# Kernel tuning notes

Hardware: AMD Instinct MI355X
Metric: run time of the kernel (lower is better)

The kernel has to match this reference:

```python
import jax, jax.numpy as jnp
import numpy as np

N, IN_DIM, OUT_DIM, H = 1024, 128, 128, 4
D = OUT_DIM // H  # head_dim = 32
NEG_SLOPE = 0.2
MASK_VAL = -1e9
LN_EPS = 1e-5


def setup_inputs() -> dict:
    key = jax.random.key(0)
    k = jax.random.split(key, 8)
    h = jax.random.normal(k[0], (N, IN_DIM), dtype=jnp.float32)
    adj = jax.random.randint(k[1], (N, N), 0, 2, dtype=jnp.int32)
    adj = adj.at[jnp.arange(N), jnp.arange(N)].set(1)  # self-loops
    s = 1.0 / np.sqrt(IN_DIM)
    W_l = jax.random.normal(k[2], (IN_DIM, OUT_DIM), dtype=jnp.float32) * s
    W_r = jax.random.normal(k[3], (IN_DIM, OUT_DIM), dtype=jnp.float32) * s
    W_v = jax.random.normal(k[4], (IN_DIM, OUT_DIM), dtype=jnp.float32) * s
    a = jax.random.normal(k[5], (D,), dtype=jnp.float32) * (1.0 / np.sqrt(D))
    ln_g = jnp.ones((OUT_DIM,), dtype=jnp.float32)
    ln_b = jnp.zeros((OUT_DIM,), dtype=jnp.float32)
    return {"h": h, "adj": adj, "W_l": W_l, "W_r": W_r, "W_v": W_v,
            "a": a, "ln_g": ln_g, "ln_b": ln_b}


def reference(h, adj, W_l, W_r, W_v, a, ln_g, ln_b):
    n = h.shape[0]
    Wlh = (h @ W_l).reshape(n, H, D)   # [N,H,D]
    Wrh = (h @ W_r).reshape(n, H, D)   # [N,H,D]
    # pairwise additive scores: pair[i,j,h,d] = Wlh[i] + Wrh[j]
    pair = Wlh[:, None, :, :] + Wrh[None, :, :, :]          # [N,N,H,D]
    pair = jnp.where(pair >= 0, pair, NEG_SLOPE * pair)      # leaky_relu(0.2)
    e = jnp.einsum('ijhd,d->ijh', pair, a)                   # [N,N,H]
    mask = (adj != 0)[:, :, None]                            # [N,N,1]
    e = jnp.where(mask, e, MASK_VAL)
    alpha = jax.nn.softmax(e, axis=1)                        # softmax over j
    v = (h @ W_v).reshape(n, H, D)                           # [N,H,D]
    agg = jnp.einsum('ijh,jhd->ihd', alpha, v).reshape(n, OUT_DIM)
    mu = jnp.mean(agg, axis=-1, keepdims=True)
    var = jnp.mean((agg - mu) ** 2, axis=-1, keepdims=True)
    y = (agg - mu) * jax.lax.rsqrt(var + LN_EPS) * ln_g + ln_b
    return jax.nn.relu(y)
```

## Files before the change

kernel.cpp:

```cpp
#include <hip/hip_runtime.h>

typedef _Float16 f16;
typedef _Float16 f16x2 __attribute__((ext_vector_type(2)));
typedef _Float16 f16x4 __attribute__((ext_vector_type(4)));
typedef _Float16 f16x8 __attribute__((ext_vector_type(8)));
typedef float    f32x4 __attribute__((ext_vector_type(4)));
typedef unsigned int u32;

#define LOG2E 1.44269504088896340736f

__device__ __forceinline__ f16x2 habs2(f16x2 v) {
    union { f16x2 h; u32 u; } x; x.h = v; x.u &= 0x7FFF7FFFu; return x.h;
}
#if __has_builtin(__builtin_amdgcn_fdot2)
__device__ __forceinline__ float fdot2f(f16x2 a, f16x2 b, float c) {
    return __builtin_amdgcn_fdot2(a, b, c, false);
}
#else
__device__ __forceinline__ float fdot2f(f16x2 a, f16x2 b, float c) {
    return c + (float)a.x * (float)b.x + (float)a.y * (float)b.y;
}
#endif
#if __has_builtin(__builtin_amdgcn_exp2f)
#define EXP2F __builtin_amdgcn_exp2f
#else
#define EXP2F exp2f
#endif

__global__ __launch_bounds__(384) void k1_proj(
        const float* __restrict__ h,  const float* __restrict__ Wl,
        const float* __restrict__ Wr, const float* __restrict__ Wv,
        f16* __restrict__ Wlh, f16* __restrict__ WrL, f16* __restrict__ VL) {
    __shared__ float hs[2][128];
    const int t = threadIdx.x, i0 = blockIdx.x * 2;
    if (t < 256) hs[t >> 7][t & 127] = h[(i0 + (t >> 7)) * 128 + (t & 127)];
    __syncthreads();

    const int wsel = t >> 7, col = t & 127;
    const float* W = (wsel == 0) ? Wl : ((wsel == 1) ? Wr : Wv);
    float a0 = 0.f, a1 = 0.f;
    #pragma unroll 16
    for (int k = 0; k < 128; k++) {
        float wv = W[k * 128 + col];
        a0 += hs[0][k] * wv;
        a1 += hs[1][k] * wv;
    }
    float accs[2] = {a0, a1};
    const int hh = col >> 5, dd = col & 31, c = dd >> 2, l = dd & 3;
    #pragma unroll
    for (int i = 0; i < 2; i++) {
        int j = i0 + i;
        f16 hv = (f16)accs[i];
        if (wsel == 0)      Wlh[j * 128 + col] = hv;
        else if (wsel == 1) WrL[((hh * 8 + c) * 1024 + j) * 4 + l] = hv;
        else                VL[(hh * 32 + dd) * 1024 + j] = hv;
    }
}

__global__ __launch_bounds__(256) void GATv2Layer_84447646974220_kernel(
        const f16* __restrict__ Wlh, const f16* __restrict__ WrL,
        const f16* __restrict__ VL,  const int* __restrict__ adj,
        const float* __restrict__ a_, const float* __restrict__ ln_g,
        const float* __restrict__ ln_b, float* __restrict__ out) {

    __shared__ __align__(16) f16 ep[4][2][1024];
    __shared__ float aggS[2][4][32];

    const int t    = threadIdx.x;
    const int lane = t & 63;
    const int hh   = t >> 6;
    const int i0   = blockIdx.x * 2;

    f16x2 p2[16], q2[16];
    #pragma unroll
    for (int d2 = 0; d2 < 16; d2++) {
        float a0 = a_[2 * d2], a1 = a_[2 * d2 + 1];
        f16x2 p; p.x = (f16)(0.6f * a0); p.y = (f16)(0.6f * a1);
        f16x2 q; q.x = (f16)(0.4f * a0); q.y = (f16)(0.4f * a1);
        p2[d2] = p; q2[d2] = q;
    }
    f16x2 wl2[2][16];
    #pragma unroll
    for (int ii = 0; ii < 2; ii++) {
        const f16x2* src = (const f16x2*)(Wlh + (i0 + ii) * 128 + hh * 32);
        #pragma unroll
        for (int c2 = 0; c2 < 16; c2++) wl2[ii][c2] = src[c2];
    }

    float maxE[2] = {-__builtin_inff(), -__builtin_inff()};
    f16x4 wrA[8], wrB[8];
    int   amA[2], amB[2];

    #pragma unroll
    for (int c = 0; c < 8; c++)
        wrA[c] = *(const f16x4*)(WrL + ((hh * 8 + c) * 1024 + lane) * 4);
    amA[0] = adj[(i0 + 0) * 1024 + lane];
    amA[1] = adj[(i0 + 1) * 1024 + lane];

    #pragma unroll
    for (int jb = 0; jb < 16; jb++) {
        const bool even = (jb & 1) == 0;
        f16x4* cur = even ? wrA : wrB;
        int*   amc = even ? amA : amB;
        f16x4* nxt = even ? wrB : wrA;
        int*   amn = even ? amB : amA;
        if (jb < 15) {
            int jn = (jb + 1) * 64 + lane;
            #pragma unroll
            for (int c = 0; c < 8; c++)
                nxt[c] = *(const f16x4*)(WrL + ((hh * 8 + c) * 1024 + jn) * 4);
            amn[0] = adj[(i0 + 0) * 1024 + jn];
            amn[1] = adj[(i0 + 1) * 1024 + jn];
        }
        int j = jb * 64 + lane;
        float e[2] = {0.f, 0.f};
        #pragma unroll
        for (int c = 0; c < 8; c++) {
            #pragma unroll
            for (int ii = 0; ii < 2; ii++) {
                f16x2 t0 = wl2[ii][2 * c]     + cur[c].lo;
                f16x2 t1 = wl2[ii][2 * c + 1] + cur[c].hi;
                e[ii] = fdot2f(p2[2 * c],     t0, e[ii]);
                e[ii] = fdot2f(q2[2 * c],     habs2(t0), e[ii]);
                e[ii] = fdot2f(p2[2 * c + 1], t1, e[ii]);
                e[ii] = fdot2f(q2[2 * c + 1], habs2(t1), e[ii]);
            }
        }
        #pragma unroll
        for (int ii = 0; ii < 2; ii++) {
            float v = amc[ii] ? e[ii] : -__builtin_inff();
            maxE[ii] = fmaxf(maxE[ii], v);
            ep[hh][ii][j] = (f16)v;
        }
    }

    float lr[2];
    #pragma unroll
    for (int ii = 0; ii < 2; ii++) {
        float M = maxE[ii];
        #pragma unroll
        for (int off = 32; off > 0; off >>= 1) M = fmaxf(M, __shfl_xor(M, off));
        float l = 0.f;
        #pragma unroll
        for (int g = 0; g < 2; g++) {
            f16x8 v = *(f16x8*)&ep[hh][ii][lane * 16 + g * 8];
            float pb[8];
            #pragma unroll
            for (int e = 0; e < 8; e++) pb[e] = EXP2F(((float)v[e] - M) * LOG2E);
            #pragma unroll
            for (int e = 0; e < 8; e++) { v[e] = (f16)pb[e]; l += pb[e]; }
            *(f16x8*)&ep[hh][ii][lane * 16 + g * 8] = v;
        }
        #pragma unroll
        for (int off = 32; off > 0; off >>= 1) l += __shfl_xor(l, off);
        lr[ii] = 1.0f / l;
    }

    f32x4 acc0 = {0.f, 0.f, 0.f, 0.f}, acc1 = {0.f, 0.f, 0.f, 0.f};
    const int q8  = (lane >> 4) << 3;
    const int m1  = lane & 1;
    const int n15 = lane & 15;
    const f16* vb = VL + (hh * 32 + n15) * 1024;

    f16x8 b0C = *(const f16x8*)(vb + q8);
    f16x8 b1C = *(const f16x8*)(vb + 16384 + q8);
    #pragma unroll
    for (int s = 0; s < 32; s++) {
        int ko = s * 32 + q8;
        f16x8 af = *(const f16x8*)&ep[hh][m1][ko];
        if (s < 31) {
            int koN = ko + 32;
            f16x8 b0N = *(const f16x8*)(vb + koN);
            f16x8 b1N = *(const f16x8*)(vb + 16384 + koN);
            acc0 = __builtin_amdgcn_mfma_f32_16x16x32_f16(af, b0C, acc0, 0, 0, 0);
            acc1 = __builtin_amdgcn_mfma_f32_16x16x32_f16(af, b1C, acc1, 0, 0, 0);
            b0C = b0N; b1C = b1N;
        } else {
            acc0 = __builtin_amdgcn_mfma_f32_16x16x32_f16(af, b0C, acc0, 0, 0, 0);
            acc1 = __builtin_amdgcn_mfma_f32_16x16x32_f16(af, b1C, acc1, 0, 0, 0);
        }
    }

    if (lane < 16) {
        aggS[0][hh][lane]      = acc0[0] * lr[0];
        aggS[0][hh][16 + lane] = acc1[0] * lr[0];
        aggS[1][hh][lane]      = acc0[1] * lr[1];
        aggS[1][hh][16 + lane] = acc1[1] * lr[1];
    }
    __syncthreads();

    if (t < 128) {
        const int node = t >> 6, ln2 = t & 63;
        float x0 = aggS[node][ln2 >> 5][ln2 & 31];
        float x1 = aggS[node][2 + (ln2 >> 5)][ln2 & 31];
        float s = x0 + x1, sq = x0 * x0 + x1 * x1;
        #pragma unroll
        for (int off = 32; off > 0; off >>= 1) {
            s  += __shfl_xor(s, off);
            sq += __shfl_xor(sq, off);
        }
        float mean = s * (1.f / 128.f);
        float var  = sq * (1.f / 128.f) - mean * mean;
        float rs   = rsqrtf(var + 1e-5f);
        float y0 = fmaxf((x0 - mean) * rs * ln_g[ln2]      + ln_b[ln2],      0.f);
        float y1 = fmaxf((x1 - mean) * rs * ln_g[ln2 + 64] + ln_b[ln2 + 64], 0.f);
        out[(i0 + node) * 128 + ln2]      = y0;
        out[(i0 + node) * 128 + 64 + ln2] = y1;
    }
}

extern "C" void kernel_launch(void* const* d_in, const int* in_sizes, int n_in,
                              void* d_out, int out_size, void* d_ws, size_t ws_size,
                              hipStream_t stream) {
    const float* h   = (const float*)d_in[0];
    const int*   adj = (const int*)d_in[1];
    const float* Wl  = (const float*)d_in[2];
    const float* Wr  = (const float*)d_in[3];
    const float* Wv  = (const float*)d_in[4];
    const float* a_  = (const float*)d_in[5];
    const float* g_  = (const float*)d_in[6];
    const float* b_  = (const float*)d_in[7];
    float* out = (float*)d_out;

    char* ws = (char*)d_ws;
    f16* Wlh = (f16*)(ws);
    f16* WrL = (f16*)(ws + 262144);
    f16* VL  = (f16*)(ws + 524288);

    k1_proj<<<512, 384, 0, stream>>>(h, Wl, Wr, Wv, Wlh, WrL, VL);
    GATv2Layer_84447646974220_kernel<<<512, 256, 0, stream>>>(
        Wlh, WrL, VL, adj, a_, g_, b_, out);
}
```

Before: 102.3 us.

## Split neighbor range across two wave groups and restructure score computation

The attention kernel now launches 512 threads per block, and each of two halves of the waves handles half of the 1024 neighbors. Per-half max and sum are combined through shared memory with extra barriers, and the partial aggregations are summed before the layer norm. The Wr projection layout changes to a row-contiguous per-head layout so each lane loads 32 halfs with four 16-byte loads. The leaky-relu dot now accumulates the linear and absolute parts separately in float and mixes them with 0.6/0.4 at the end. The goal is more waves in flight and shorter serial loops per wave, at the cost of extra synchronization and register pressure under the 512-thread launch bound.

New measurement: 103.3 us. About the same (+0.9%).

```diff
diff --git a/kernel.cpp b/kernel.cpp
--- a/kernel.cpp
+++ b/kernel.cpp
@@ -2,7 +2,6 @@
 
 typedef _Float16 f16;
 typedef _Float16 f16x2 __attribute__((ext_vector_type(2)));
-typedef _Float16 f16x4 __attribute__((ext_vector_type(4)));
 typedef _Float16 f16x8 __attribute__((ext_vector_type(8)));
 typedef float    f32x4 __attribute__((ext_vector_type(4)));
 typedef unsigned int u32;
@@ -30,7 +29,7 @@
 __global__ __launch_bounds__(384) void k1_proj(
         const float* __restrict__ h,  const float* __restrict__ Wl,
         const float* __restrict__ Wr, const float* __restrict__ Wv,
-        f16* __restrict__ Wlh, f16* __restrict__ WrL, f16* __restrict__ VL) {
+        f16* __restrict__ Wlh, f16* __restrict__ WrR, f16* __restrict__ VL) {
     __shared__ float hs[2][128];
     const int t = threadIdx.x, i0 = blockIdx.x * 2;
     if (t < 256) hs[t >> 7][t & 127] = h[(i0 + (t >> 7)) * 128 + (t & 127)];
@@ -46,38 +45,40 @@
         a1 += hs[1][k] * wv;
     }
     float accs[2] = {a0, a1};
-    const int hh = col >> 5, dd = col & 31, c = dd >> 2, l = dd & 3;
+    const int hh = col >> 5, dd = col & 31;
     #pragma unroll
     for (int i = 0; i < 2; i++) {
         int j = i0 + i;
         f16 hv = (f16)accs[i];
         if (wsel == 0)      Wlh[j * 128 + col] = hv;
-        else if (wsel == 1) WrL[((hh * 8 + c) * 1024 + j) * 4 + l] = hv;
+        else if (wsel == 1) WrR[(hh * 1024 + j) * 32 + dd] = hv;
         else                VL[(hh * 32 + dd) * 1024 + j] = hv;
     }
 }
 
-__global__ __launch_bounds__(256) void GATv2Layer_84447646974220_kernel(
-        const f16* __restrict__ Wlh, const f16* __restrict__ WrL,
+__global__ __launch_bounds__(512, 4) void GATv2Layer_84447646974220_kernel(
+        const f16* __restrict__ Wlh, const f16* __restrict__ WrR,
         const f16* __restrict__ VL,  const int* __restrict__ adj,
         const float* __restrict__ a_, const float* __restrict__ ln_g,
         const float* __restrict__ ln_b, float* __restrict__ out) {
 
     __shared__ __align__(16) f16 ep[4][2][1024];
-    __shared__ float aggS[2][4][32];
+    __shared__ float aggS[2][2][128];
+    __shared__ float redM[2][4][2];
+    __shared__ float redS[2][4][2];
 
     const int t    = threadIdx.x;
     const int lane = t & 63;
-    const int hh   = t >> 6;
+    const int w    = t >> 6;
+    const int hh   = w & 3;
+    const int half = w >> 2;
     const int i0   = blockIdx.x * 2;
 
-    f16x2 p2[16], q2[16];
+    f16x2 a2[16];
     #pragma unroll
     for (int d2 = 0; d2 < 16; d2++) {
-        float a0 = a_[2 * d2], a1 = a_[2 * d2 + 1];
-        f16x2 p; p.x = (f16)(0.6f * a0); p.y = (f16)(0.6f * a1);
-        f16x2 q; q.x = (f16)(0.4f * a0); q.y = (f16)(0.4f * a1);
-        p2[d2] = p; q2[d2] = q;
+        f16x2 v; v.x = (f16)a_[2 * d2]; v.y = (f16)a_[2 * d2 + 1];
+        a2[d2] = v;
     }
     f16x2 wl2[2][16];
     #pragma unroll
@@ -87,91 +88,97 @@
         for (int c2 = 0; c2 < 16; c2++) wl2[ii][c2] = src[c2];
     }
 
+    union V64 { f16x8 v8[4]; f16x2 v2[16]; };
+    V64 wA, wB; int amA[2], amB[2];
     float maxE[2] = {-__builtin_inff(), -__builtin_inff()};
-    f16x4 wrA[8], wrB[8];
-    int   amA[2], amB[2];
-
-    #pragma unroll
-    for (int c = 0; c < 8; c++)
-        wrA[c] = *(const f16x4*)(WrL + ((hh * 8 + c) * 1024 + lane) * 4);
-    amA[0] = adj[(i0 + 0) * 1024 + lane];
-    amA[1] = adj[(i0 + 1) * 1024 + lane];
-
-    #pragma unroll
-    for (int jb = 0; jb < 16; jb++) {
+    const f16* wbase = WrR + hh * 32768;
+
+    {
+        int j0 = half * 512 + lane;
+        #pragma unroll
+        for (int k = 0; k < 4; k++)
+            wA.v8[k] = *(const f16x8*)(wbase + j0 * 32 + k * 8);
+        amA[0] = adj[(i0 + 0) * 1024 + j0];
+        amA[1] = adj[(i0 + 1) * 1024 + j0];
+    }
+    #pragma unroll
+    for (int jb = 0; jb < 8; jb++) {
         const bool even = (jb & 1) == 0;
-        f16x4* cur = even ? wrA : wrB;
-        int*   amc = even ? amA : amB;
-        f16x4* nxt = even ? wrB : wrA;
-        int*   amn = even ? amB : amA;
-        if (jb < 15) {
-            int jn = (jb + 1) * 64 + lane;
+        V64& cur = even ? wA : wB;
+        int* amc = even ? amA : amB;
+        V64& nxt = even ? wB : wA;
+        int* amn = even ? amB : amA;
+        if (jb < 7) {
+            int jn = half * 512 + (jb + 1) * 64 + lane;
             #pragma unroll
-            for (int c = 0; c < 8; c++)
-                nxt[c] = *(const f16x4*)(WrL + ((hh * 8 + c) * 1024 + jn) * 4);
+            for (int k = 0; k < 4; k++)
+                nxt.v8[k] = *(const f16x8*)(wbase + jn * 32 + k * 8);
             amn[0] = adj[(i0 + 0) * 1024 + jn];
             amn[1] = adj[(i0 + 1) * 1024 + jn];
         }
-        int j = jb * 64 + lane;
-        float e[2] = {0.f, 0.f};
-        #pragma unroll
-        for (int c = 0; c < 8; c++) {
+        int j = half * 512 + jb * 64 + lane;
+        #pragma unroll
+        for (int ii = 0; ii < 2; ii++) {
+            float lin = 0.f, ab = 0.f;
             #pragma unroll
-            for (int ii = 0; ii < 2; ii++) {
-                f16x2 t0 = wl2[ii][2 * c]     + cur[c].lo;
-                f16x2 t1 = wl2[ii][2 * c + 1] + cur[c].hi;
-                e[ii] = fdot2f(p2[2 * c],     t0, e[ii]);
-                e[ii] = fdot2f(q2[2 * c],     habs2(t0), e[ii]);
-                e[ii] = fdot2f(p2[2 * c + 1], t1, e[ii]);
-                e[ii] = fdot2f(q2[2 * c + 1], habs2(t1), e[ii]);
+            for (int p = 0; p < 16; p++) {
+                f16x2 t2 = wl2[ii][p] + cur.v2[p];
+                lin = fdot2f(a2[p], t2, lin);
+                ab  = fdot2f(a2[p], habs2(t2), ab);
             }
-        }
-        #pragma unroll
-        for (int ii = 0; ii < 2; ii++) {
-            float v = amc[ii] ? e[ii] : -__builtin_inff();
+            float e = 0.6f * lin + 0.4f * ab;
+            float v = amc[ii] ? e : -__builtin_inff();
             maxE[ii] = fmaxf(maxE[ii], v);
             ep[hh][ii][j] = (f16)v;
         }
     }
 
-    float lr[2];
     #pragma unroll
     for (int ii = 0; ii < 2; ii++) {
         float M = maxE[ii];
         #pragma unroll
         for (int off = 32; off > 0; off >>= 1) M = fmaxf(M, __shfl_xor(M, off));
-        float l = 0.f;
-        #pragma unroll
-        for (int g = 0; g < 2; g++) {
-            f16x8 v = *(f16x8*)&ep[hh][ii][lane * 16 + g * 8];
-            float pb[8];
-            #pragma unroll
-            for (int e = 0; e < 8; e++) pb[e] = EXP2F(((float)v[e] - M) * LOG2E);
-            #pragma unroll
-            for (int e = 0; e < 8; e++) { v[e] = (f16)pb[e]; l += pb[e]; }
-            *(f16x8*)&ep[hh][ii][lane * 16 + g * 8] = v;
-        }
+        if (lane == 0) redM[half][hh][ii] = M;
+    }
+    __syncthreads();
+
+    #pragma unroll
+    for (int ii = 0; ii < 2; ii++) {
+        float M = fmaxf(redM[0][hh][ii], redM[1][hh][ii]);
+        f16x8 v = *(f16x8*)&ep[hh][ii][half * 512 + lane * 8];
+        float pb[8], l = 0.f;
+        #pragma unroll
+        for (int e = 0; e < 8; e++) pb[e] = EXP2F(((float)v[e] - M) * LOG2E);
+        #pragma unroll
+        for (int e = 0; e < 8; e++) { v[e] = (f16)pb[e]; l += pb[e]; }
+        *(f16x8*)&ep[hh][ii][half * 512 + lane * 8] = v;
         #pragma unroll
         for (int off = 32; off > 0; off >>= 1) l += __shfl_xor(l, off);
-        lr[ii] = 1.0f / l;
-    }
+        if (lane == 0) redS[half][hh][ii] = l;
+    }
+    __syncthreads();
+
+    float lr[2];
+    #pragma unroll
+    for (int ii = 0; ii < 2; ii++)
+        lr[ii] = 1.0f / (redS[0][hh][ii] + redS[1][hh][ii]);
 
     f32x4 acc0 = {0.f, 0.f, 0.f, 0.f}, acc1 = {0.f, 0.f, 0.f, 0.f};
     const int q8  = (lane >> 4) << 3;
     const int m1  = lane & 1;
     const int n15 = lane & 15;
     const f16* vb = VL + (hh * 32 + n15) * 1024;
-
-    f16x8 b0C = *(const f16x8*)(vb + q8);
-    f16x8 b1C = *(const f16x8*)(vb + 16384 + q8);
-    #pragma unroll
-    for (int s = 0; s < 32; s++) {
-        int ko = s * 32 + q8;
+    const int kbase = half * 512;
+
+    f16x8 b0C = *(const f16x8*)(vb + kbase + q8);
+    f16x8 b1C = *(const f16x8*)(vb + 16384 + kbase + q8);
+    #pragma unroll
+    for (int s = 0; s < 16; s++) {
+        int ko = kbase + s * 32 + q8;
         f16x8 af = *(const f16x8*)&ep[hh][m1][ko];
-        if (s < 31) {
-            int koN = ko + 32;
-            f16x8 b0N = *(const f16x8*)(vb + koN);
-            f16x8 b1N = *(const f16x8*)(vb + 16384 + koN);
+        if (s < 15) {
+            f16x8 b0N = *(const f16x8*)(vb + ko + 32);
+            f16x8 b1N = *(const f16x8*)(vb + 16384 + ko + 32);
             acc0 = __builtin_amdgcn_mfma_f32_16x16x32_f16(af, b0C, acc0, 0, 0, 0);
             acc1 = __builtin_amdgcn_mfma_f32_16x16x32_f16(af, b1C, acc1, 0, 0, 0);
             b0C = b0N; b1C = b1N;
@@ -182,17 +189,17 @@
     }
 
     if (lane < 16) {
-        aggS[0][hh][lane]      = acc0[0] * lr[0];
-        aggS[0][hh][16 + lane] = acc1[0] * lr[0];
-        aggS[1][hh][lane]      = acc0[1] * lr[1];
-        aggS[1][hh][16 + lane] = acc1[1] * lr[1];
+        aggS[half][0][hh * 32 + lane]      = acc0[0] * lr[0];
+        aggS[half][0][hh * 32 + 16 + lane] = acc1[0] * lr[0];
+        aggS[half][1][hh * 32 + lane]      = acc0[1] * lr[1];
+        aggS[half][1][hh * 32 + 16 + lane] = acc1[1] * lr[1];
     }
     __syncthreads();
 
     if (t < 128) {
-        const int node = t >> 6, ln2 = t & 63;
-        float x0 = aggS[node][ln2 >> 5][ln2 & 31];
-        float x1 = aggS[node][2 + (ln2 >> 5)][ln2 & 31];
+        const int node = t >> 6, c = t & 63;
+        float x0 = aggS[0][node][c]      + aggS[1][node][c];
+        float x1 = aggS[0][node][c + 64] + aggS[1][node][c + 64];
         float s = x0 + x1, sq = x0 * x0 + x1 * x1;
         #pragma unroll
         for (int off = 32; off > 0; off >>= 1) {
@@ -202,10 +209,10 @@
         float mean = s * (1.f / 128.f);
         float var  = sq * (1.f / 128.f) - mean * mean;
         float rs   = rsqrtf(var + 1e-5f);
-        float y0 = fmaxf((x0 - mean) * rs * ln_g[ln2]      + ln_b[ln2],      0.f);
-        float y1 = fmaxf((x1 - mean) * rs * ln_g[ln2 + 64] + ln_b[ln2 + 64], 0.f);
-        out[(i0 + node) * 128 + ln2]      = y0;
-        out[(i0 + node) * 128 + 64 + ln2] = y1;
+        float y0 = fmaxf((x0 - mean) * rs * ln_g[c]      + ln_b[c],      0.f);
+        float y1 = fmaxf((x1 - mean) * rs * ln_g[c + 64] + ln_b[c + 64], 0.f);
+        out[(i0 + node) * 128 + c]      = y0;
+        out[(i0 + node) * 128 + 64 + c] = y1;
     }
 }
 
@@ -224,10 +231,10 @@
 
     char* ws = (char*)d_ws;
     f16* Wlh = (f16*)(ws);
-    f16* WrL = (f16*)(ws + 262144);
+    f16* WrR = (f16*)(ws + 262144);
     f16* VL  = (f16*)(ws + 524288);
 
-    k1_proj<<<512, 384, 0, stream>>>(h, Wl, Wr, Wv, Wlh, WrL, VL);
-    GATv2Layer_84447646974220_kernel<<<512, 256, 0, stream>>>(
-        Wlh, WrL, VL, adj, a_, g_, b_, out);
-}
+    k1_proj<<<512, 384, 0, stream>>>(h, Wl, Wr, Wv, Wlh, WrR, VL);
+    GATv2Layer_84447646974220_kernel<<<512, 512, 0, stream>>>(
+        Wlh, WrR, VL, adj, a_, g_, b_, out);
+}
```
